# Kernel optimization log

Hardware: AMD Instinct MI355X
Metric: run time of the kernel (lower is better)

Reference implementation:

```python
import jax, jax.numpy as jnp
import numpy as np

D_MODEL, NUM_HEADS, D_FF = 1024, 16, 4096
HEAD_DIM = D_MODEL // NUM_HEADS
EPS = 1e-5


def _layernorm(x, g, b):
    m = jnp.mean(x, axis=-1, keepdims=True)
    v = jnp.mean((x - m) ** 2, axis=-1, keepdims=True)
    return (x - m) * jax.lax.rsqrt(v + EPS) * g + b


def setup_inputs() -> dict:
    key = jax.random.key(0)
    ks = jax.random.split(key, 16)
    N, S = 4, 2048
    x = jax.random.normal(ks[0], (N, S, D_MODEL), dtype=jnp.float32)
    # mask broadcastable against energy of shape (N, S, H, H) -- see notes: code
    # computes per-position head-vs-head attention, not SxS attention.
    mask = jax.random.randint(ks[1], (N, 1, 1, NUM_HEADS), 0, 2, dtype=jnp.int32)
    s = 0.02
    return {
        "x": x,
        "Wqkv": jax.random.normal(ks[2], (D_MODEL, 3 * D_MODEL), dtype=jnp.float32) * s,
        "bqkv": jnp.zeros((3 * D_MODEL,), jnp.float32),
        "Wo": jax.random.normal(ks[3], (D_MODEL, D_MODEL), dtype=jnp.float32) * s,
        "bo": jnp.zeros((D_MODEL,), jnp.float32),
        "g1": jnp.ones((D_MODEL,), jnp.float32),
        "beta1": jnp.zeros((D_MODEL,), jnp.float32),
        "W1": jax.random.normal(ks[4], (D_MODEL, D_FF), dtype=jnp.float32) * s,
        "bf1": jnp.zeros((D_FF,), jnp.float32),
        "W2": jax.random.normal(ks[5], (D_FF, D_MODEL), dtype=jnp.float32) * s,
        "bf2": jnpp if False else jnp.zeros((D_MODEL,), jnp.float32),
        "g2": jnp.ones((D_MODEL,), jnp.float32),
        "beta2": jnp.zeros((D_MODEL,), jnp.float32),
        "mask": mask,
    }


def reference(x, Wqkv, bqkv, Wo, bo, g1, beta1, W1, bf1, W2, bf2, g2, beta2, mask):
    N, S, D = x.shape
    H, hd = NUM_HEADS, HEAD_DIM
    # fused QKV projection
    qkv = (x @ Wqkv + bqkv).reshape(N, S, 3, H, hd).transpose(2, 0, 3, 1, 4)
    q, k, v = qkv[0], qkv[1], qkv[2]  # each (N, H, S, hd)
    # faithful to torch einsum 'nqhd,nkhd->nhqk' on (N,H,S,hd) operands:
    # energy[n,s,i,j] = sum_d q[n,i,s,d] * k[n,j,s,d]  -> (N, S, H, H)
    energy = jnp.einsum('nise,njse->nsij', q, k)
    energy = jnp.where(mask == 0, jnp.float32(-1e20), energy)
    attn = jax.nn.softmax(energy / np.sqrt(hd).astype(np.float32), axis=3)
    # torch einsum 'nhql,nlhd->nqhd': out[n,i,s,d] = sum_l attn[n,s,i,l]*v[n,l,s,d]
    out = jnp.einsum('nsil,nlse->nise', attn, v)  # (N, H, S, hd)
    out = out.reshape(N, S, D)  # row-major flatten, exactly as torch .reshape
    attn_out = out @ Wo + bo
    h = _layernorm(attn_out + x, g1, beta1)
    ff = jax.nn.relu(h @ W1 + bf1) @ W2 + bf2  # dropout = identity (eval)
    return _layernorm(ff + h, g2, beta2)
```

## Files before the change

kernel.cpp:

```cpp
#include <hip/hip_runtime.h>
#include <cstdint>
#include <cstddef>


using f32x4  = __attribute__((ext_vector_type(4))) float;
using bf16x8 = __attribute__((ext_vector_type(8))) __bf16;

__device__ __forceinline__ unsigned short f2b(float f) {
  union { float f; uint32_t u; } v; v.f = f;
  uint32_t r = v.u + 0x7FFFu + ((v.u >> 16) & 1u);
  return (unsigned short)(r >> 16);
}
__device__ __forceinline__ float b2f(unsigned short u) {
  union { uint32_t u; float f; } v; v.u = ((uint32_t)u) << 16;
  return v.f;
}

__device__ __forceinline__ void gload_lds16(const unsigned short* g,
                                            unsigned short* l) {
  __builtin_amdgcn_global_load_lds(
      (const __attribute__((address_space(1))) unsigned int*)g,
      (__attribute__((address_space(3))) unsigned int*)l, 16, 0, 0);
}

#define MEMBAR() asm volatile("" ::: "memory")
__device__ __forceinline__ void barrier_raw() {
  MEMBAR();
  __builtin_amdgcn_s_barrier();
  MEMBAR();
}
template <int N>
__device__ __forceinline__ void vmwait() {
  if constexpr (N == 6)      asm volatile("s_waitcnt vmcnt(6)" ::: "memory");
  else if constexpr (N == 5) asm volatile("s_waitcnt vmcnt(5)" ::: "memory");
  else                       asm volatile("s_waitcnt vmcnt(0)" ::: "memory");
}

__global__ __launch_bounds__(256) void transpose_cvt_kernel(
    const float* __restrict__ W, unsigned short* __restrict__ WT, int K, int N) {
  __shared__ float tile[32][33];
  const int j0 = blockIdx.x * 32, k0 = blockIdx.y * 32;
  const int tx = threadIdx.x, ty = threadIdx.y;
#pragma unroll
  for (int i = 0; i < 4; ++i)
    tile[ty + 8 * i][tx] = W[(size_t)(k0 + ty + 8 * i) * N + j0 + tx];
  __syncthreads();
#pragma unroll
  for (int i = 0; i < 4; ++i)
    WT[(size_t)(j0 + ty + 8 * i) * K + k0 + tx] = f2b(tile[tx][ty + 8 * i]);
}

__global__ __launch_bounds__(256) void cvt_bf16_kernel(
    const float* __restrict__ in, unsigned short* __restrict__ out, int n4) {
  for (int i = blockIdx.x * blockDim.x + threadIdx.x; i < n4;
       i += gridDim.x * blockDim.x) {
    float4 v = ((const float4*)in)[i];
    uint32_t lo = (uint32_t)f2b(v.x) | ((uint32_t)f2b(v.y) << 16);
    uint32_t hi = (uint32_t)f2b(v.z) | ((uint32_t)f2b(v.w) << 16);
    ((uint2*)out)[i] = make_uint2(lo, hi);
  }
}

template <int BN, bool SPLITK, bool OUTB, bool RELU>
__global__ __launch_bounds__(512, 2) void gemm8p_kernel(
    const unsigned short* __restrict__ A, const unsigned short* __restrict__ B,
    const float* __restrict__ bias, void* __restrict__ C,
    unsigned short* __restrict__ C2, int M, int N, int Ks, int Kd, int nbn) {
  constexpr int NF   = BN / 128;
  constexpr int WN   = BN / 8;
  constexpr int BH   = BN / 2;
  constexpr int BIS  = BN / 128;
  constexpr int INF  = 4 + BN / 128;
  constexpr int ASTR = (256 + BN) * 64;

  __shared__ unsigned short lds[2 * ASTR];

  const int tid  = threadIdx.x;
  const int lane = tid & 63, wave = tid >> 6;
  const int wm = wave >> 2, wn = wave & 3;
  const int lr = lane & 15, lk = lane >> 4;
  const int x7 = lr & 7;

  const int nwg = gridDim.x, cpx = nwg >> 3, id = blockIdx.x;
  const int wg = (id & 7) * cpx + (id >> 3);
  int bm, bn, sk;
  if (SPLITK) { bm = wg >> 3; bn = (wg & 7) >> 1; sk = wg & 1; }
  else        { bm = wg / nbn; bn = wg % nbn; sk = 0; }

  const unsigned short* Ab = A + (size_t)bm * 256 * Ks + (size_t)sk * Kd;
  const unsigned short* Bb = B + (size_t)bn * BN * Ks + (size_t)sk * Kd;

  const int srow = tid >> 3;
  const int scol = ((tid & 7) ^ (srow & 7)) * 8;
  const int ldst = wave * 8 * 64;

  const int NT = Kd >> 6;

  f32x4 acc[8][2 * NF] = {};
  bf16x8 aF[4][2], b0F[NF][2], b1F[NF][2];

  auto stA = [&](int t, int h, int b) {
#pragma unroll
    for (int i = 0; i < 2; ++i)
      gload_lds16(Ab + (size_t)(h * 128 + i * 64 + srow) * Ks + t * 64 + scol,
                  &lds[b * ASTR + (h * 128 + i * 64) * 64 + ldst]);
  };
  auto stB = [&](int t, int h, int b) {
#pragma unroll
    for (int i = 0; i < BIS; ++i)
      gload_lds16(Bb + (size_t)(h * BH + i * 64 + srow) * Ks + t * 64 + scol,
                  &lds[b * ASTR + 256 * 64 + (h * BH + i * 64) * 64 + ldst]);
  };
  auto rdA = [&](int b, int mh) {
#pragma unroll
    for (int mi = 0; mi < 4; ++mi) {
      int r = mh * 128 + wm * 64 + mi * 16 + lr;
#pragma unroll
      for (int kk = 0; kk < 2; ++kk)
        aF[mi][kk] = *(const bf16x8*)
            &lds[b * ASTR + r * 64 + ((kk * 4 + lk) ^ x7) * 8];
    }
  };
  auto rdB = [&](int b, int nh, bf16x8 (&bF)[NF][2]) {
#pragma unroll
    for (int ni = 0; ni < NF; ++ni) {
      int r = nh * BH + wn * WN + ni * 16 + lr;
#pragma unroll
      for (int kk = 0; kk < 2; ++kk)
        bF[ni][kk] = *(const bf16x8*)
            &lds[b * ASTR + 256 * 64 + r * 64 + ((kk * 4 + lk) ^ x7) * 8];
    }
  };
  auto mmQ = [&](bf16x8 (&bF)[NF][2], int mh, int nh) {
    __builtin_amdgcn_s_setprio(1);
#pragma unroll
    for (int mi = 0; mi < 4; ++mi)
#pragma unroll
      for (int ni = 0; ni < NF; ++ni)
#pragma unroll
        for (int kk = 0; kk < 2; ++kk)
          acc[mh * 4 + mi][nh * NF + ni] = __builtin_amdgcn_mfma_f32_16x16x32_bf16(
              aF[mi][kk], bF[ni][kk], acc[mh * 4 + mi][nh * NF + ni], 0, 0, 0);
    __builtin_amdgcn_s_setprio(0);
  };

  stA(0, 0, 0); stB(0, 0, 0); stA(0, 1, 0); stB(0, 1, 0);
  stA(1, 0, 1); stB(1, 0, 1); stA(1, 1, 1);
  vmwait<INF>();
  barrier_raw();

  for (int t = 0; t < NT; ++t) {
    const int b = t & 1;
    const bool s1 = (t + 1 < NT), s2 = (t + 2 < NT);
    rdA(b, 0);
    rdB(b, 0, b0F);
    if (s1) stB(t + 1, 1, b ^ 1);
    barrier_raw();
    mmQ(b0F, 0, 0);
    barrier_raw();
    rdB(b, 1, b1F);
    if (s2) stA(t + 2, 0, b);
    barrier_raw();
    mmQ(b1F, 0, 1);
    barrier_raw();
    rdA(b, 1);
    if (s2) stB(t + 2, 0, b);
    barrier_raw();
    mmQ(b1F, 1, 1);
    barrier_raw();
    if (s2) {
      stA(t + 2, 1, b);
      vmwait<INF>();
    } else if (s1) {
      vmwait<0>();
    }
    barrier_raw();
    mmQ(b0F, 1, 0);
    barrier_raw();
  }

  const int orow0 = bm * 256 + wm * 64;
  const int ocol0 = bn * BN + wn * WN;
#pragma unroll
  for (int mh = 0; mh < 2; ++mh)
#pragma unroll
    for (int nh = 0; nh < 2; ++nh)
#pragma unroll
      for (int ni = 0; ni < NF; ++ni) {
        int col = ocol0 + nh * BH + ni * 16 + lr;
        float bv = bias[col];
#pragma unroll
        for (int mi = 0; mi < 4; ++mi)
#pragma unroll
          for (int r = 0; r < 4; ++r) {
            int row = orow0 + mh * 128 + mi * 16 + lk * 4 + r;
            float val = acc[mh * 4 + mi][nh * NF + ni][r];
            if (SPLITK) {
              if (sk == 0)
                ((float*)C)[(size_t)row * N + col] = val + bv;
              else
                C2[(size_t)row * N + col] = f2b(val);
            } else {
              val += bv;
              if (RELU) val = fmaxf(val, 0.f);
              if (OUTB)
                ((unsigned short*)C)[(size_t)row * N + col] = f2b(val);
              else
                ((float*)C)[(size_t)row * N + col] = val;
            }
          }
      }
}

__global__ __launch_bounds__(256) void attn_kernel(
    const unsigned short* __restrict__ qkv, const int* __restrict__ mask,
    unsigned short* __restrict__ outb) {
  __shared__ float sq[16][68], sk[16][68], sv[16][68];
  __shared__ float sp[16][17];
  const int pos = blockIdx.x;
  const int n = pos >> 11, s = pos & 2047;
  const int tid = threadIdx.x;
  const unsigned short* row = qkv + (size_t)pos * 3072;
#pragma unroll
  for (int it = 0; it < 3; ++it) {
    uint2 raw = *(const uint2*)(row + it * 1024 + tid * 4);
    float f0 = b2f((unsigned short)(raw.x & 0xffffu));
    float f1 = b2f((unsigned short)(raw.x >> 16));
    float f2 = b2f((unsigned short)(raw.y & 0xffffu));
    float f3 = b2f((unsigned short)(raw.y >> 16));
    float(*dst)[68] = (it == 0) ? sq : (it == 1) ? sk : sv;
    int r = tid >> 4, d = (tid & 15) * 4;
    dst[r][d] = f0; dst[r][d + 1] = f1; dst[r][d + 2] = f2; dst[r][d + 3] = f3;
  }
  __syncthreads();
  {
    const int i = tid >> 4, j = tid & 15;
    float e = 0.f;
#pragma unroll
    for (int d = 0; d < 64; d += 4) {
      float4 qa = *(const float4*)&sq[i][d];
      float4 kb = *(const float4*)&sk[j][d];
      e += qa.x * kb.x + qa.y * kb.y + qa.z * kb.z + qa.w * kb.w;
    }
    if (mask[n * 16 + j] == 0) e = -1e20f;
    e *= 0.125f;
    float mx = e;
#pragma unroll
    for (int o = 8; o > 0; o >>= 1) mx = fmaxf(mx, __shfl_xor(mx, o, 16));
    float pe = __expf(e - mx);
    float sm = pe;
#pragma unroll
    for (int o = 8; o > 0; o >>= 1) sm += __shfl_xor(sm, o, 16);
    sp[i][j] = pe / sm;
  }
  __syncthreads();
  {
    const int w = tid >> 6, d = tid & 63;
    float o0 = 0, o1 = 0, o2 = 0, o3 = 0;
#pragma unroll
    for (int l = 0; l < 16; ++l) {
      float vv = sv[l][d];
      o0 += sp[w][l] * vv;      o1 += sp[w + 4][l] * vv;
      o2 += sp[w + 8][l] * vv;  o3 += sp[w + 12][l] * vv;
    }
    outb[(((size_t)n * 16 + w     ) * 2048 + s) * 64 + d] = f2b(o0);
    outb[(((size_t)n * 16 + w + 4 ) * 2048 + s) * 64 + d] = f2b(o1);
    outb[(((size_t)n * 16 + w + 8 ) * 2048 + s) * 64 + d] = f2b(o2);
    outb[(((size_t)n * 16 + w + 12) * 2048 + s) * 64 + d] = f2b(o3);
  }
}

__global__ __launch_bounds__(256) void ln_kernel(
    const float* __restrict__ A, const unsigned short* __restrict__ P2,
    const float* __restrict__ R,
    const float* __restrict__ g, const float* __restrict__ be,
    float* __restrict__ outf, unsigned short* __restrict__ outb) {
  const int row = blockIdx.x, tid = threadIdx.x;
  const size_t base = (size_t)row * 1024 + tid * 4;
  float4 a = *(const float4*)(A + base);
  float4 r = *(const float4*)(R + base);
  float x0 = a.x + r.x, x1 = a.y + r.y, x2 = a.z + r.z, x3 = a.w + r.w;
  if (P2) {
    uint2 p = *(const uint2*)(P2 + base);
    x0 += b2f((unsigned short)(p.x & 0xffffu));
    x1 += b2f((unsigned short)(p.x >> 16));
    x2 += b2f((unsigned short)(p.y & 0xffffu));
    x3 += b2f((unsigned short)(p.y >> 16));
  }
  float s = x0 + x1 + x2 + x3;
#pragma unroll
  for (int o = 32; o > 0; o >>= 1) s += __shfl_xor(s, o);
  __shared__ float red[4];
  const int lane = tid & 63, wv = tid >> 6;
  if (lane == 0) red[wv] = s;
  __syncthreads();
  float mean = (red[0] + red[1] + red[2] + red[3]) * (1.f / 1024.f);
  float d0 = x0 - mean, d1 = x1 - mean, d2 = x2 - mean, d3 = x3 - mean;
  float q = d0 * d0 + d1 * d1 + d2 * d2 + d3 * d3;
#pragma unroll
  for (int o = 32; o > 0; o >>= 1) q += __shfl_xor(q, o);
  __syncthreads();
  if (lane == 0) red[wv] = q;
  __syncthreads();
  float var = (red[0] + red[1] + red[2] + red[3]) * (1.f / 1024.f);
  float rs = rsqrtf(var + 1e-5f);
  const int col = tid * 4;
  float4 gv = *(const float4*)(g + col);
  float4 bv = *(const float4*)(be + col);
  float y0 = d0 * rs * gv.x + bv.x;
  float y1 = d1 * rs * gv.y + bv.y;
  float y2 = d2 * rs * gv.z + bv.z;
  float y3 = d3 * rs * gv.w + bv.w;
  *(float4*)(outf + base) = make_float4(y0, y1, y2, y3);
  if (outb) {
    uint32_t lo = (uint32_t)f2b(y0) | ((uint32_t)f2b(y1) << 16);
    uint32_t hi = (uint32_t)f2b(y2) | ((uint32_t)f2b(y3) << 16);
    *(uint2*)(outb + base) = make_uint2(lo, hi);
  }
}

extern "C" void kernel_launch(void* const* d_in, const int* in_sizes, int n_in,
                              void* d_out, int out_size, void* d_ws,
                              size_t ws_size, hipStream_t stream) {
  (void)in_sizes; (void)n_in; (void)out_size; (void)ws_size;
  const float* x     = (const float*)d_in[0];
  const float* Wqkv  = (const float*)d_in[1];
  const float* bqkv  = (const float*)d_in[2];
  const float* Wo    = (const float*)d_in[3];
  const float* bo    = (const float*)d_in[4];
  const float* g1    = (const float*)d_in[5];
  const float* beta1 = (const float*)d_in[6];
  const float* W1    = (const float*)d_in[7];
  const float* bf1   = (const float*)d_in[8];
  const float* W2    = (const float*)d_in[9];
  const float* bf2   = (const float*)d_in[10];
  const float* g2    = (const float*)d_in[11];
  const float* beta2 = (const float*)d_in[12];
  const int*   mask  = (const int*)d_in[13];
  float* out = (float*)d_out;

  char* ws = (char*)d_ws;
  unsigned short* WqkvT = (unsigned short*)(ws + 0);
  unsigned short* WoT   = (unsigned short*)(ws + 6291456);
  unsigned short* W1T   = (unsigned short*)(ws + 8388608);
  unsigned short* W2T   = (unsigned short*)(ws + 16777216);
  unsigned short* xb    = (unsigned short*)(ws + 25165824);
  float*          h_f   = (float*)(ws + 41943040);
  unsigned short* h_b   = (unsigned short*)(ws + 75497472);
  float*          ao2   = (float*)(ws + 92274688);
  unsigned short* qkvb  = (unsigned short*)(ws + 125829120);
  unsigned short* aob   = (unsigned short*)(ws + 176160768);
  unsigned short* ff1   = qkvb;
  float*          ff2   = ao2;
  unsigned short* ff2p2 = xb;

  transpose_cvt_kernel<<<dim3(96, 32),  dim3(32, 8), 0, stream>>>(Wqkv, WqkvT, 1024, 3072);
  transpose_cvt_kernel<<<dim3(32, 32),  dim3(32, 8), 0, stream>>>(Wo,   WoT,   1024, 1024);
  transpose_cvt_kernel<<<dim3(128, 32), dim3(32, 8), 0, stream>>>(W1,   W1T,   1024, 4096);
  transpose_cvt_kernel<<<dim3(32, 128), dim3(32, 8), 0, stream>>>(W2,   W2T,   4096, 1024);
  cvt_bf16_kernel<<<2048, 256, 0, stream>>>(x, xb, 8192 * 1024 / 4);

  gemm8p_kernel<256, false, true, false><<<dim3(32 * 12), 512, 0, stream>>>(
      xb, WqkvT, bqkv, qkvb, nullptr, 8192, 3072, 1024, 1024, 12);
  attn_kernel<<<8192, 256, 0, stream>>>(qkvb, mask, aob);
  gemm8p_kernel<128, false, false, false><<<dim3(32 * 8), 512, 0, stream>>>(
      aob, WoT, bo, ao2, nullptr, 8192, 1024, 1024, 1024, 8);
  ln_kernel<<<8192, 256, 0, stream>>>(ao2, nullptr, x, g1, beta1, h_f, h_b);
  gemm8p_kernel<256, false, true, true><<<dim3(32 * 16), 512, 0, stream>>>(
      h_b, W1T, bf1, ff1, nullptr, 8192, 4096, 1024, 1024, 16);
  gemm8p_kernel<256, true, false, false><<<dim3(32 * 8), 512, 0, stream>>>(
      ff1, W2T, bf2, ff2, ff2p2, 8192, 1024, 4096, 2048, 4);
  ln_kernel<<<8192, 256, 0, stream>>>(ff2, ff2p2, h_f, g2, beta2, out, nullptr);
}
```

Baseline: 329.8 us.

## Restructure GEMM main loop to prefetch next-tile fragments and refine vmcnt waits

Rewrites the bf16 GEMM K-loop as a manually unrolled pair of iterations in which the A and B register fragments for the next K tile are read from LDS during the current tile's MFMA phases. Global-to-LDS load order and per-phase vmcnt wait counts are recomputed so each phase waits only for the data it needs, and the last two iterations are peeled. The aim is to hide LDS read latency behind matrix math and relax global-load waits. The cost is more fragment registers, which risks register pressure at two workgroups per CU, and the loop now assumes NT is even and at least 2.

Result: slower. 695.8 us (+110.9%).

```diff
diff --git a/kernel.cpp b/kernel.cpp
--- a/kernel.cpp
+++ b/kernel.cpp
@@ -31,9 +31,20 @@
 }
 template <int N>
 __device__ __forceinline__ void vmwait() {
-  if constexpr (N == 6)      asm volatile("s_waitcnt vmcnt(6)" ::: "memory");
-  else if constexpr (N == 5) asm volatile("s_waitcnt vmcnt(5)" ::: "memory");
-  else                       asm volatile("s_waitcnt vmcnt(0)" ::: "memory");
+  static_assert(N >= 0 && N <= 12, "vmcnt range");
+  if constexpr (N == 0)  asm volatile("s_waitcnt vmcnt(0)" ::: "memory");
+  if constexpr (N == 1)  asm volatile("s_waitcnt vmcnt(1)" ::: "memory");
+  if constexpr (N == 2)  asm volatile("s_waitcnt vmcnt(2)" ::: "memory");
+  if constexpr (N == 3)  asm volatile("s_waitcnt vmcnt(3)" ::: "memory");
+  if constexpr (N == 4)  asm volatile("s_waitcnt vmcnt(4)" ::: "memory");
+  if constexpr (N == 5)  asm volatile("s_waitcnt vmcnt(5)" ::: "memory");
+  if constexpr (N == 6)  asm volatile("s_waitcnt vmcnt(6)" ::: "memory");
+  if constexpr (N == 7)  asm volatile("s_waitcnt vmcnt(7)" ::: "memory");
+  if constexpr (N == 8)  asm volatile("s_waitcnt vmcnt(8)" ::: "memory");
+  if constexpr (N == 9)  asm volatile("s_waitcnt vmcnt(9)" ::: "memory");
+  if constexpr (N == 10) asm volatile("s_waitcnt vmcnt(10)" ::: "memory");
+  if constexpr (N == 11) asm volatile("s_waitcnt vmcnt(11)" ::: "memory");
+  if constexpr (N == 12) asm volatile("s_waitcnt vmcnt(12)" ::: "memory");
 }
 
 __global__ __launch_bounds__(256) void transpose_cvt_kernel(
@@ -69,9 +80,16 @@
   constexpr int NF   = BN / 128;
   constexpr int WN   = BN / 8;
   constexpr int BH   = BN / 2;
-  constexpr int BIS  = BN / 128;
-  constexpr int INF  = 4 + BN / 128;
+  constexpr int SA   = 2;
+  constexpr int SB   = NF;
   constexpr int ASTR = (256 + BN) * 64;
+  constexpr int W1  = 2 * SA + 2 * SB;
+  constexpr int W2  = 2 * SA + 3 * SB;
+  constexpr int W3  = 2 * SA + 3 * SB;
+  constexpr int W4  = 3 * SA + 2 * SB;
+  constexpr int W2a = SA + 2 * SB;
+  constexpr int W3a = SA + SB;
+  constexpr int W4a = SA;
 
   __shared__ unsigned short lds[2 * ASTR];
 
@@ -97,87 +115,91 @@
   const int NT = Kd >> 6;
 
   f32x4 acc[8][2 * NF] = {};
-  bf16x8 aF[4][2], b0F[NF][2], b1F[NF][2];
-
-  auto stA = [&](int t, int h, int b) {
-#pragma unroll
-    for (int i = 0; i < 2; ++i)
-      gload_lds16(Ab + (size_t)(h * 128 + i * 64 + srow) * Ks + t * 64 + scol,
-                  &lds[b * ASTR + (h * 128 + i * 64) * 64 + ldst]);
-  };
-  auto stB = [&](int t, int h, int b) {
-#pragma unroll
-    for (int i = 0; i < BIS; ++i)
-      gload_lds16(Bb + (size_t)(h * BH + i * 64 + srow) * Ks + t * 64 + scol,
-                  &lds[b * ASTR + 256 * 64 + (h * BH + i * 64) * 64 + ldst]);
-  };
-  auto rdA = [&](int b, int mh) {
-#pragma unroll
-    for (int mi = 0; mi < 4; ++mi) {
-      int r = mh * 128 + wm * 64 + mi * 16 + lr;
-#pragma unroll
-      for (int kk = 0; kk < 2; ++kk)
-        aF[mi][kk] = *(const bf16x8*)
-            &lds[b * ASTR + r * 64 + ((kk * 4 + lk) ^ x7) * 8];
-    }
-  };
-  auto rdB = [&](int b, int nh, bf16x8 (&bF)[NF][2]) {
-#pragma unroll
-    for (int ni = 0; ni < NF; ++ni) {
-      int r = nh * BH + wn * WN + ni * 16 + lr;
-#pragma unroll
-      for (int kk = 0; kk < 2; ++kk)
-        bF[ni][kk] = *(const bf16x8*)
-            &lds[b * ASTR + 256 * 64 + r * 64 + ((kk * 4 + lk) ^ x7) * 8];
-    }
-  };
-  auto mmQ = [&](bf16x8 (&bF)[NF][2], int mh, int nh) {
-    __builtin_amdgcn_s_setprio(1);
-#pragma unroll
-    for (int mi = 0; mi < 4; ++mi)
-#pragma unroll
-      for (int ni = 0; ni < NF; ++ni)
-#pragma unroll
-        for (int kk = 0; kk < 2; ++kk)
-          acc[mh * 4 + mi][nh * NF + ni] = __builtin_amdgcn_mfma_f32_16x16x32_bf16(
-              aF[mi][kk], bF[ni][kk], acc[mh * 4 + mi][nh * NF + ni], 0, 0, 0);
-    __builtin_amdgcn_s_setprio(0);
-  };
-
-  stA(0, 0, 0); stB(0, 0, 0); stA(0, 1, 0); stB(0, 1, 0);
-  stA(1, 0, 1); stB(1, 0, 1); stA(1, 1, 1);
-  vmwait<INF>();
+  bf16x8 a0[4][2], a1[4][2], b0[NF][2], b0n[NF][2], b1[NF][2];
+
+#define STA(T, H, BUF)                                                        \
+  _Pragma("unroll") for (int i_ = 0; i_ < 2; ++i_)                            \
+      gload_lds16(Ab + (size_t)((H)*128 + i_ * 64 + srow) * Ks + (T)*64 + scol,\
+                  &lds[(BUF)*ASTR + ((H)*128 + i_ * 64) * 64 + ldst])
+#define STB(T, H, BUF)                                                        \
+  _Pragma("unroll") for (int i_ = 0; i_ < SB; ++i_)                           \
+      gload_lds16(Bb + (size_t)((H)*BH + i_ * 64 + srow) * Ks + (T)*64 + scol, \
+                  &lds[(BUF)*ASTR + 256 * 64 + ((H)*BH + i_ * 64) * 64 + ldst])
+#define RDA(BUF, H, DST)                                                      \
+  _Pragma("unroll") for (int mi_ = 0; mi_ < 4; ++mi_)                         \
+    _Pragma("unroll") for (int kk_ = 0; kk_ < 2; ++kk_)                       \
+      DST[mi_][kk_] = *(const bf16x8*)&lds[(BUF)*ASTR +                       \
+          ((H)*128 + wm * 64 + mi_ * 16 + lr) * 64 + ((kk_ * 4 + lk) ^ x7) * 8]
+#define RDB(BUF, H, DST)                                                      \
+  _Pragma("unroll") for (int ni_ = 0; ni_ < NF; ++ni_)                        \
+    _Pragma("unroll") for (int kk_ = 0; kk_ < 2; ++kk_)                       \
+      DST[ni_][kk_] = *(const bf16x8*)&lds[(BUF)*ASTR + 256 * 64 +            \
+          ((H)*BH + wn * WN + ni_ * 16 + lr) * 64 + ((kk_ * 4 + lk) ^ x7) * 8]
+#define MMQ(AS, BS, MH, NH)                                                   \
+  do {                                                                        \
+    __builtin_amdgcn_s_setprio(1);                                            \
+    _Pragma("unroll") for (int mi_ = 0; mi_ < 4; ++mi_)                       \
+      _Pragma("unroll") for (int ni_ = 0; ni_ < NF; ++ni_)                    \
+        _Pragma("unroll") for (int kk_ = 0; kk_ < 2; ++kk_)                   \
+          acc[(MH)*4 + mi_][(NH)*NF + ni_] =                                  \
+              __builtin_amdgcn_mfma_f32_16x16x32_bf16(                        \
+                  AS[mi_][kk_], BS[ni_][kk_],                                 \
+                  acc[(MH)*4 + mi_][(NH)*NF + ni_], 0, 0, 0);                 \
+    __builtin_amdgcn_s_setprio(0);                                            \
+  } while (0)
+
+#define GITER(T, BRD, BWR, Wp1, Wp2, Wp3, Wp4, ST, RDN)                       \
+  do {                                                                        \
+    const int b_ = (T)&1;                                                     \
+                                    \
+    RDB(b_, 1, b1);                                                           \
+    vmwait<Wp1>();                                                            \
+    barrier_raw();                                                            \
+    MMQ(a0, BRD, 0, 0);                                                       \
+    barrier_raw();                                                            \
+                 \
+    RDA(b_, 1, a1);                                                           \
+    if (ST) { STA((T) + 2, 0, b_); STB((T) + 2, 0, b_); }                     \
+    vmwait<Wp2>();                                                            \
+    barrier_raw();                                                            \
+    MMQ(a0, b1, 0, 1);                                                        \
+    barrier_raw();                                                            \
+                   \
+    if (RDN) RDA(b_ ^ 1, 0, a0);                                              \
+    if (ST) STB((T) + 2, 1, b_);                                              \
+    vmwait<Wp3>();                                                            \
+    barrier_raw();                                                            \
+    MMQ(a1, b1, 1, 1);                                                        \
+    barrier_raw();                                                            \
+                  \
+    if (RDN) RDB(b_ ^ 1, 0, BWR);                                             \
+    if (ST) STA((T) + 2, 1, b_);                                              \
+    vmwait<Wp4>();                                                            \
+    barrier_raw();                                                            \
+    MMQ(a1, BRD, 1, 0);                                                       \
+    barrier_raw();                                                            \
+  } while (0)
+
+  STA(0, 0, 0); STB(0, 0, 0); STB(0, 1, 0); STA(0, 1, 0);
+  STA(1, 0, 1); STB(1, 0, 1); STB(1, 1, 1); STA(1, 1, 1);
+  vmwait<3 * SA + 2 * SB>();
   barrier_raw();
-
-  for (int t = 0; t < NT; ++t) {
-    const int b = t & 1;
-    const bool s1 = (t + 1 < NT), s2 = (t + 2 < NT);
-    rdA(b, 0);
-    rdB(b, 0, b0F);
-    if (s1) stB(t + 1, 1, b ^ 1);
-    barrier_raw();
-    mmQ(b0F, 0, 0);
-    barrier_raw();
-    rdB(b, 1, b1F);
-    if (s2) stA(t + 2, 0, b);
-    barrier_raw();
-    mmQ(b1F, 0, 1);
-    barrier_raw();
-    rdA(b, 1);
-    if (s2) stB(t + 2, 0, b);
-    barrier_raw();
-    mmQ(b1F, 1, 1);
-    barrier_raw();
-    if (s2) {
-      stA(t + 2, 1, b);
-      vmwait<INF>();
-    } else if (s1) {
-      vmwait<0>();
-    }
-    barrier_raw();
-    mmQ(b0F, 1, 0);
-    barrier_raw();
-  }
+  RDA(0, 0, a0);
+  RDB(0, 0, b0);
+
+  for (int tt = 0; tt + 4 <= NT; tt += 2) {
+    GITER(tt,     b0,  b0n, W1, W2,  W3,  W4,  true,  true);
+    GITER(tt + 1, b0n, b0,  W1, W2,  W3,  W4,  true,  true);
+  }
+  GITER(NT - 2, b0,  b0n, W1, W2a, W3a, W4a, false, true);
+  GITER(NT - 1, b0n, b0,  0,  0,   0,   0,   false, false);
+
+#undef GITER
+#undef MMQ
+#undef RDA
+#undef RDB
+#undef STA
+#undef STB
 
   const int orow0 = bm * 256 + wm * 64;
   const int ocol0 = bn * BN + wn * WN;
```
